# Performance work log

Hardware: AMD Instinct MI355X
Metric: run time of the kernel (lower is better)

Reference implementation:

```python
import jax, jax.numpy as jnp
import numpy as np

N_NODES = 100000
N_EDGES = 1600000
N_GRAPHS = 512
IN_CH = 128
FILT = 128
N_CONVS = 4  # 1 + n_rounds(3)


def setup_inputs() -> dict:
    key = jax.random.key(0)
    ks = jax.random.split(key, 10)
    x = jax.random.normal(ks[0], (N_NODES, IN_CH), dtype=jnp.float32)
    edge_index = jax.random.randint(ks[1], (2, N_EDGES), 0, N_NODES, dtype=jnp.int32)
    batch = jnp.sort(jax.random.randint(ks[2], (N_NODES,), 0, N_GRAPHS, dtype=jnp.int32))
    # GCNConv weights (in_channels == filter_size so all convs stack uniformly)
    s = 1.0 / np.sqrt(FILT)
    conv_w = jax.random.uniform(ks[3], (N_CONVS, IN_CH, FILT), jnp.float32, -s, s)
    conv_b = jnp.zeros((N_CONVS, FILT), jnp.float32)
    fc1_w = jax.random.uniform(ks[4], (FILT, FILT), jnp.float32, -s, s)
    fc1_b = jax.random.uniform(ks[5], (FILT,), jnp.float32, -s, s)
    fc2_w = jax.random.uniform(ks[6], (FILT, 1), jnp.float32, -s, s)
    fc2_b = jax.random.uniform(ks[7], (1,), jnp.float32, -s, s)
    return {"x": x, "edge_index": edge_index, "batch": batch, "batch_size": N_GRAPHS,
            "conv_w": conv_w, "conv_b": conv_b,
            "fc1_w": fc1_w, "fc1_b": fc1_b, "fc2_w": fc2_w, "fc2_b": fc2_b}


def _gcn_layer(x, W, b, src, dst, dinv):
    # GCNConv with improved=True: A_hat = A + 2I, sym-normalized by D_hat^{-1/2}
    h = x @ W                                   # [N, F]
    enorm = dinv[src] * dinv[dst]               # [E]
    agg = jax.ops.segment_sum(h[src] * enorm[:, None], dst, num_segments=N_NODES)
    self_loop = (2.0 * dinv * dinv)[:, None] * h
    return agg + self_loop + b


def reference(x, edge_index, batch, batch_size, conv_w, conv_b, fc1_w, fc1_b, fc2_w, fc2_b):
    src, dst = edge_index[0], edge_index[1]
    # degree including improved self-loop weight 2
    deg = jax.ops.segment_sum(jnp.ones((N_EDGES,), x.dtype), dst, num_segments=N_NODES) + 2.0
    dinv = jax.lax.rsqrt(deg)
    for i in range(N_CONVS):
        x = _gcn_layer(x, conv_w[i], conv_b[i], src, dst, dinv)
        x = jax.nn.relu(x)
        # dropout is identity in eval mode
    # global mean pool over graphs
    sums = jax.ops.segment_sum(x, batch, num_segments=batch_size)
    cnt = jax.ops.segment_sum(jnp.ones((N_NODES,), x.dtype), batch, num_segments=batch_size)
    pooled = sums / jnp.maximum(cnt, 1.0)[:, None]   # [G, F]
    h = jax.nn.relu(pooled @ fc1_w + fc1_b)
    out = h @ fc2_w + fc2_b                          # [G, 1]
    return out[:, 0]
```

## Files before the change

kernel.cpp:

```cpp
#include <hip/hip_runtime.h>
#include <hip/hip_fp16.h>

#define N_NODES 100000
#define N_EDGES 1600000
#define N_GRAPHS 512
#define F 128
#define N_CONVS 4
#define SCAN_NBLK ((N_NODES + 1023) / 1024)

#define SUBW 256
#define SUBW_NODES 391
#define SCAP 7040
#define ACHUNK 4096
#define BINA_BLOCKS ((N_EDGES + ACHUNK - 1) / ACHUNK)
#define EBUF 8192

#define W2_STRIDE 132
#define W2_LAYER (128 * W2_STRIDE)

typedef __attribute__((ext_vector_type(8))) short short8;
typedef __attribute__((ext_vector_type(4))) float f32x4;

union FragU { uint4 u; short8 v; };
union HU4 { uint4 u; __half2 h[4]; };

__device__ __forceinline__ unsigned int pack_hilo(float f) {
    unsigned int u = __float_as_uint(f);
    unsigned int hb = u & 0xFFFF0000u;
    float d = f - __uint_as_float(hb);
    unsigned int lb = __float_as_uint(d) >> 16;
    return (u >> 16) | (lb << 16);
}


__global__ void dinv_kernel(const int* __restrict__ cnt, float* __restrict__ dinv) {
    int n = blockIdx.x * blockDim.x + threadIdx.x;
    if (n < N_NODES) dinv[n] = rsqrtf((float)cnt[n] + 2.0f);
}

__global__ void scan1_kernel(const int* __restrict__ cnt, int* __restrict__ excl,
                             int* __restrict__ blksum) {
    __shared__ int sums[256];
    int t = threadIdx.x;
    int base = blockIdx.x * 1024 + t * 4;
    int v0 = 0, v1 = 0, v2 = 0, v3 = 0;
    if (base + 0 < N_NODES) v0 = cnt[base + 0];
    if (base + 1 < N_NODES) v1 = cnt[base + 1];
    if (base + 2 < N_NODES) v2 = cnt[base + 2];
    if (base + 3 < N_NODES) v3 = cnt[base + 3];
    int s = v0 + v1 + v2 + v3;
    sums[t] = s;
    __syncthreads();
    for (int off = 1; off < 256; off <<= 1) {
        int y = (t >= off) ? sums[t - off] : 0;
        __syncthreads();
        sums[t] += y;
        __syncthreads();
    }
    int pre = sums[t] - s;
    if (base + 0 < N_NODES) excl[base + 0] = pre;
    if (base + 1 < N_NODES) excl[base + 1] = pre + v0;
    if (base + 2 < N_NODES) excl[base + 2] = pre + v0 + v1;
    if (base + 3 < N_NODES) excl[base + 3] = pre + v0 + v1 + v2;
    if (t == 255) blksum[blockIdx.x] = sums[255];
}

__global__ void scan2_kernel(int* __restrict__ blksum, int nblk) {
    __shared__ int sh[128];
    int t = threadIdx.x;
    int v = (t < nblk) ? blksum[t] : 0;
    sh[t] = v;
    __syncthreads();
    for (int off = 1; off < 128; off <<= 1) {
        int y = (t >= off) ? sh[t - off] : 0;
        __syncthreads();
        sh[t] += y;
        __syncthreads();
    }
    if (t < nblk) blksum[t] = sh[t] - v;
}

__global__ void scan3_kernel(int* __restrict__ rowptr, const int* __restrict__ blksum) {
    int t = threadIdx.x;
    int base = blockIdx.x * 1024 + t * 4;
    int off = blksum[blockIdx.x];
#pragma unroll
    for (int i = 0; i < 4; i++) {
        int idx = base + i;
        if (idx < N_NODES) rowptr[idx] += off;
    }
    if (blockIdx.x == 0 && t == 0) rowptr[N_NODES] = N_EDGES;
}


__global__ __launch_bounds__(256) void binA_kernel(
        const int* __restrict__ src, const int* __restrict__ dst,
        int* __restrict__ cursor, int2* __restrict__ staging) {
    __shared__ int2 buf[ACHUNK];
    __shared__ int cnt_s[SUBW], off_s[SUBW], cur_s[SUBW], gb_s[SUBW], sh[SUBW];
    int t = threadIdx.x;
    cnt_s[t] = 0;
    __syncthreads();

    int base = blockIdx.x * ACHUNK;
    int n = N_EDGES - base;
    if (n > ACHUNK) n = ACHUNK;

    for (int li = t; li < n; li += 256)
        atomicAdd(&cnt_s[dst[base + li] / SUBW_NODES], 1);
    __syncthreads();

    int v = cnt_s[t];
    sh[t] = v;
    __syncthreads();
    for (int off = 1; off < SUBW; off <<= 1) {
        int y = (t >= off) ? sh[t - off] : 0;
        __syncthreads();
        sh[t] += y;
        __syncthreads();
    }
    int excl = sh[t] - v;
    off_s[t] = excl;
    cur_s[t] = excl;
    gb_s[t] = atomicAdd(&cursor[t], v);
    __syncthreads();

    for (int li = t; li < n; li += 256) {
        int e = base + li;
        int d = dst[e], s = src[e];
        int p = atomicAdd(&cur_s[d / SUBW_NODES], 1);
        buf[p] = make_int2(s, d);
    }
    __syncthreads();

    for (int i = t; i < n; i += 256) {
        int2 e = buf[i];
        int w = e.y / SUBW_NODES;
        int idx = gb_s[w] + (i - off_s[w]);
        if (idx < SCAP) staging[(size_t)w * SCAP + idx] = e;
    }
}

__global__ __launch_bounds__(256) void subcount_kernel(
        const int2* __restrict__ staging, const int* __restrict__ cursor,
        int* __restrict__ cnt) {
    __shared__ int hist[SUBW_NODES];
    int b = blockIdx.x, t = threadIdx.x;
    int n0 = b * SUBW_NODES;
    int n1 = n0 + SUBW_NODES;
    if (n1 > N_NODES) n1 = N_NODES;
    int nn = n1 - n0;
    for (int i = t; i < nn; i += 256) hist[i] = 0;
    __syncthreads();
    int m = cursor[b];
    if (m > SCAP) m = SCAP;
    for (int i = t; i < m; i += 256) {
        int d = staging[(size_t)b * SCAP + i].y;
        atomicAdd(&hist[d - n0], 1);
    }
    __syncthreads();
    for (int i = t; i < nn; i += 256) cnt[n0 + i] = hist[i];
}

__global__ __launch_bounds__(512) void binB_kernel(
        const int2* __restrict__ staging, const int* __restrict__ cursor,
        const int* __restrict__ rowptr, const float* __restrict__ dinv,
        int2* __restrict__ edges) {
    __shared__ int rowl[SUBW_NODES + 1];
    __shared__ int lcur[SUBW_NODES];
    __shared__ int2 ebuf[EBUF];
    int b = blockIdx.x, t = threadIdx.x;
    int n0 = b * SUBW_NODES;
    int n1 = n0 + SUBW_NODES;
    if (n1 > N_NODES) n1 = N_NODES;
    int nn = n1 - n0;

    for (int i = t; i <= nn; i += 512) rowl[i] = rowptr[n0 + i];
    for (int i = t; i < nn; i += 512) lcur[i] = 0;
    __syncthreads();

    int gb = rowl[0];
    int total = rowl[nn] - gb;
    int m = cursor[b];
    if (m > SCAP) m = SCAP;

    for (int i = t; i < m; i += 512) {
        int2 e = staging[(size_t)b * SCAP + i];
        int s = e.x, d = e.y;
        float wt = dinv[s] * dinv[d];
        int dl = d - n0;
        int lpos = (rowl[dl] - gb) + atomicAdd(&lcur[dl], 1);
        if (lpos < EBUF) ebuf[lpos] = make_int2(s, __float_as_int(wt));
    }
    __syncthreads();

    for (int i = t; i < total; i += 512)
        if (i < EBUF) edges[gb + i] = ebuf[i];
}


__global__ void wpack_kernel(const float* __restrict__ conv_w, unsigned int* __restrict__ W2g) {
    int idx = blockIdx.x * 256 + threadIdx.x;
    if (idx < N_CONVS * 16384) {
        int L = idx >> 14;
        int e = idx & 16383;
        int k = e >> 7;
        int n = e & 127;
        float f = conv_w[(size_t)L * 16384 + k * 128 + n];
        W2g[(size_t)L * W2_LAYER + n * W2_STRIDE + k] = pack_hilo(f);
    }
}


template<bool F16IN>
__global__ __launch_bounds__(256, 2) void gemm_mfma_t(const void* __restrict__ Xv,
                                                      const unsigned int* __restrict__ W2g,
                                                      __half* __restrict__ Hh) {
    __shared__ unsigned int wlds[128 * W2_STRIDE];
    int t = threadIdx.x;

    {
        const uint4* s4 = (const uint4*)W2g;
        uint4* d4 = (uint4*)wlds;
#pragma unroll
        for (int i = 0; i < 17; i++) {
            int idx = i * 256 + t;
            if (idx < (128 * W2_STRIDE) / 4) d4[idx] = s4[idx];
        }
    }
    __syncthreads();

    int w = t >> 6;
    int l = t & 63;
    int m = l & 15;
    int q = l >> 4;
    int r0 = blockIdx.x * 128 + w * 32 + m;
    int r1 = r0 + 16;
    int r0c = (r0 > N_NODES - 1) ? (N_NODES - 1) : r0;
    int r1c = (r1 > N_NODES - 1) ? (N_NODES - 1) : r1;

    uint4 a0[8], a1[8];
#pragma unroll
    for (int i = 0; i < 8; i++) {
        if constexpr (F16IN) {
            const uint2* X2 = (const uint2*)Xv;
            uint2 hv = X2[(size_t)r0c * 32 + i * 4 + q];
            float2 f0 = __half22float2(*(const __half2*)&hv.x);
            float2 f1 = __half22float2(*(const __half2*)&hv.y);
            a0[i].x = pack_hilo(f0.x); a0[i].y = pack_hilo(f0.y);
            a0[i].z = pack_hilo(f1.x); a0[i].w = pack_hilo(f1.y);
            uint2 gv = X2[(size_t)r1c * 32 + i * 4 + q];
            float2 g0 = __half22float2(*(const __half2*)&gv.x);
            float2 g1 = __half22float2(*(const __half2*)&gv.y);
            a1[i].x = pack_hilo(g0.x); a1[i].y = pack_hilo(g0.y);
            a1[i].z = pack_hilo(g1.x); a1[i].w = pack_hilo(g1.y);
        } else {
            const float4* X4 = (const float4*)Xv;
            float4 xv = X4[(size_t)r0c * 32 + i * 4 + q];
            a0[i].x = pack_hilo(xv.x); a0[i].y = pack_hilo(xv.y);
            a0[i].z = pack_hilo(xv.z); a0[i].w = pack_hilo(xv.w);
            float4 yv = X4[(size_t)r1c * 32 + i * 4 + q];
            a1[i].x = pack_hilo(yv.x); a1[i].y = pack_hilo(yv.y);
            a1[i].z = pack_hilo(yv.z); a1[i].w = pack_hilo(yv.w);
        }
    }

    f32x4 acc0[8], acc1[8];
#pragma unroll
    for (int nb = 0; nb < 8; nb++) {
        acc0[nb] = (f32x4){0.f, 0.f, 0.f, 0.f};
        acc1[nb] = (f32x4){0.f, 0.f, 0.f, 0.f};
    }

#pragma unroll
    for (int nb = 0; nb < 8; nb++) {
        const unsigned int* wb = &wlds[(nb * 16 + m) * W2_STRIDE];
#pragma unroll
        for (int i = 0; i < 8; i++) {
            uint4 b = *(const uint4*)(wb + i * 16 + q * 4);
            FragU fa0, fa1, fb, fr;
            fa0.u = a0[i]; fa1.u = a1[i]; fb.u = b;
            acc0[nb] = __builtin_amdgcn_mfma_f32_16x16x32_bf16(fa0.v, fb.v, acc0[nb], 0, 0, 0);
            acc1[nb] = __builtin_amdgcn_mfma_f32_16x16x32_bf16(fa1.v, fb.v, acc1[nb], 0, 0, 0);
            fr.u.x = (b.x >> 16) | (b.x << 16);
            fr.u.y = (b.y >> 16) | (b.y << 16);
            fr.u.z = (b.z >> 16) | (b.z << 16);
            fr.u.w = (b.w >> 16) | (b.w << 16);
            acc0[nb] = __builtin_amdgcn_mfma_f32_16x16x32_bf16(fa0.v, fr.v, acc0[nb], 0, 0, 0);
            acc1[nb] = __builtin_amdgcn_mfma_f32_16x16x32_bf16(fa1.v, fr.v, acc1[nb], 0, 0, 0);
        }
    }

    int rbase = blockIdx.x * 128 + w * 32 + q * 4;
#pragma unroll
    for (int nb = 0; nb < 8; nb++) {
#pragma unroll
        for (int r = 0; r < 4; r++) {
            int row = rbase + r;
            if (row < N_NODES) Hh[(size_t)row * F + nb * 16 + m] = __float2half(acc0[nb][r]);
            int row1 = row + 16;
            if (row1 < N_NODES) Hh[(size_t)row1 * F + nb * 16 + m] = __float2half(acc1[nb][r]);
        }
    }
}


__global__ __launch_bounds__(256) void agg_kernel(const uint4* __restrict__ H16,
                                                  const int* __restrict__ rowptr,
                                                  const int2* __restrict__ edges,
                                                  const float* __restrict__ dinv,
                                                  const float4* __restrict__ bias4,
                                                  uint4* __restrict__ Xo) {
    int node = blockIdx.x * 4 + (threadIdx.x >> 6);
    if (node >= N_NODES) return;
    int lane = threadIdx.x & 63;
    int c16 = lane & 15;
    int slot = lane >> 4;

    int lo = rowptr[node];
    int hi = rowptr[node + 1];
    int him1 = hi - 1;

    float4 aL = make_float4(0.f, 0.f, 0.f, 0.f);
    float4 aH = make_float4(0.f, 0.f, 0.f, 0.f);

    for (int i = lo + slot; i < hi; i += 16) {
        int s[4]; float w[4]; uint4 v[4];
#pragma unroll
        for (int j = 0; j < 4; j++) {
            int ij = i + 4 * j;
            int cj = (ij < him1) ? ij : him1;
            int2 e = edges[cj];
            s[j] = e.x;
            w[j] = (ij < hi) ? __int_as_float(e.y) : 0.f;
        }
#pragma unroll
        for (int j = 0; j < 4; j++) v[j] = H16[(size_t)s[j] * 16 + c16];
#pragma unroll
        for (int j = 0; j < 4; j++) {
            HU4 x; x.u = v[j];
            float2 p0 = __half22float2(x.h[0]);
            float2 p1 = __half22float2(x.h[1]);
            float2 p2 = __half22float2(x.h[2]);
            float2 p3 = __half22float2(x.h[3]);
            aL.x = fmaf(w[j], p0.x, aL.x); aL.y = fmaf(w[j], p0.y, aL.y);
            aL.z = fmaf(w[j], p1.x, aL.z); aL.w = fmaf(w[j], p1.y, aL.w);
            aH.x = fmaf(w[j], p2.x, aH.x); aH.y = fmaf(w[j], p2.y, aH.y);
            aH.z = fmaf(w[j], p3.x, aH.z); aH.w = fmaf(w[j], p3.y, aH.w);
        }
    }

    aL.x += __shfl_down(aL.x, 32, 64); aL.y += __shfl_down(aL.y, 32, 64);
    aL.z += __shfl_down(aL.z, 32, 64); aL.w += __shfl_down(aL.w, 32, 64);
    aH.x += __shfl_down(aH.x, 32, 64); aH.y += __shfl_down(aH.y, 32, 64);
    aH.z += __shfl_down(aH.z, 32, 64); aH.w += __shfl_down(aH.w, 32, 64);
    aL.x += __shfl_down(aL.x, 16, 64); aL.y += __shfl_down(aL.y, 16, 64);
    aL.z += __shfl_down(aL.z, 16, 64); aL.w += __shfl_down(aL.w, 16, 64);
    aH.x += __shfl_down(aH.x, 16, 64); aH.y += __shfl_down(aH.y, 16, 64);
    aH.z += __shfl_down(aH.z, 16, 64); aH.w += __shfl_down(aH.w, 16, 64);

    if (slot == 0) {
        float dn = dinv[node];
        float sw = 2.0f * dn * dn;
        HU4 x; x.u = H16[(size_t)node * 16 + c16];
        float2 p0 = __half22float2(x.h[0]);
        float2 p1 = __half22float2(x.h[1]);
        float2 p2 = __half22float2(x.h[2]);
        float2 p3 = __half22float2(x.h[3]);
        float4 bL = bias4[c16 * 2];
        float4 bH = bias4[c16 * 2 + 1];
        float4 rL, rH;
        rL.x = fmaxf(fmaf(sw, p0.x, aL.x) + bL.x, 0.f);
        rL.y = fmaxf(fmaf(sw, p0.y, aL.y) + bL.y, 0.f);
        rL.z = fmaxf(fmaf(sw, p1.x, aL.z) + bL.z, 0.f);
        rL.w = fmaxf(fmaf(sw, p1.y, aL.w) + bL.w, 0.f);
        rH.x = fmaxf(fmaf(sw, p2.x, aH.x) + bH.x, 0.f);
        rH.y = fmaxf(fmaf(sw, p2.y, aH.y) + bH.y, 0.f);
        rH.z = fmaxf(fmaf(sw, p3.x, aH.z) + bH.z, 0.f);
        rH.w = fmaxf(fmaf(sw, p3.y, aH.w) + bH.w, 0.f);
        HU4 o;
        o.h[0] = __floats2half2_rn(rL.x, rL.y);
        o.h[1] = __floats2half2_rn(rL.z, rL.w);
        o.h[2] = __floats2half2_rn(rH.x, rH.y);
        o.h[3] = __floats2half2_rn(rH.z, rH.w);
        Xo[(size_t)node * 16 + c16] = o.u;
    }
}


__global__ __launch_bounds__(256) void pool_fc_kernel(const __half* __restrict__ x,
                                                      const int* __restrict__ batch,
                                                      const float* __restrict__ fc1w,
                                                      const float* __restrict__ fc1b,
                                                      const float* __restrict__ fc2w,
                                                      const float* __restrict__ fc2b,
                                                      float* __restrict__ out) {
    __shared__ float part[2][F];
    __shared__ float pooled[F];
    __shared__ int bnd[2];
    __shared__ float red[2];
    int g = blockIdx.x, t = threadIdx.x;
    int c = t & 127, hlf = t >> 7;

    if (t < 2) {
        int target = g + t;
        int lo = 0, hi = N_NODES;
        while (lo < hi) {
            int m = (lo + hi) >> 1;
            if (batch[m] < target) lo = m + 1;
            else hi = m;
        }
        bnd[t] = lo;
    }
    __syncthreads();
    int lo = bnd[0], hi = bnd[1];

    float s = 0.f;
    int n = lo + hlf;
    for (; n + 6 < hi; n += 8) {
        float v0 = __half2float(x[(size_t)n * F + c]);
        float v1 = __half2float(x[(size_t)(n + 2) * F + c]);
        float v2 = __half2float(x[(size_t)(n + 4) * F + c]);
        float v3 = __half2float(x[(size_t)(n + 6) * F + c]);
        s += (v0 + v1) + (v2 + v3);
    }
    for (; n < hi; n += 2) s += __half2float(x[(size_t)n * F + c]);
    part[hlf][c] = s;
    __syncthreads();

    if (t < F) {
        float cntf = fmaxf((float)(hi - lo), 1.0f);
        pooled[c] = (part[0][c] + part[1][c]) / cntf;
    }
    __syncthreads();

    if (t < F) {
        float acc = fc1b[t];
#pragma unroll 4
        for (int k = 0; k < F; k++) acc = fmaf(pooled[k], fc1w[k * F + t], acc);
        acc = fmaxf(acc, 0.f);

        float p = acc * fc2w[t];
#pragma unroll
        for (int o = 32; o > 0; o >>= 1) p += __shfl_down(p, o, 64);
        if ((t & 63) == 0) red[t >> 6] = p;
    }
    __syncthreads();
    if (t == 0) out[g] = red[0] + red[1] + fc2b[0];
}


extern "C" void kernel_launch(void* const* d_in, const int* in_sizes, int n_in,
                              void* d_out, int out_size, void* d_ws, size_t ws_size,
                              hipStream_t stream) {
    const float* x_in   = (const float*)d_in[0];
    const int*   eidx   = (const int*)d_in[1];
    const int*   batch  = (const int*)d_in[2];
    const float* conv_w = (const float*)d_in[4];
    const float* conv_b = (const float*)d_in[5];
    const float* fc1w   = (const float*)d_in[6];
    const float* fc1b   = (const float*)d_in[7];
    const float* fc2w   = (const float*)d_in[8];
    const float* fc2b   = (const float*)d_in[9];
    float* out = (float*)d_out;

    const int* src = eidx;
    const int* dst = eidx + N_EDGES;

    char* ws = (char*)d_ws;
    size_t off = 0;
    auto alloc = [&](size_t bytes) -> char* {
        char* p = ws + off;
        off += (bytes + 255) & ~(size_t)255;
        return p;
    };
    __half* bufA  = (__half*)alloc((size_t)N_NODES * F * 2);
    __half* bufH  = (__half*)alloc((size_t)N_NODES * F * 2);
    float*  dinv  = (float*)alloc((size_t)N_NODES * 4);
    int*    cnt   = (int*)alloc((size_t)N_NODES * 4);
    int*    rowp  = (int*)alloc((size_t)(N_NODES + 1) * 4);
    int2*   edges = (int2*)alloc((size_t)N_EDGES * 8);
    unsigned int* W2g = (unsigned int*)alloc((size_t)N_CONVS * W2_LAYER * 4);
    int*    blks  = (int*)alloc(128 * 4);
    int*    cursor = (int*)alloc(SUBW * 4);
    int2*   staging = (int2*)alloc((size_t)SUBW * SCAP * 8);
    (void)ws_size; (void)in_sizes; (void)n_in; (void)out_size;

    hipMemsetAsync(cursor, 0, SUBW * 4, stream);
    binA_kernel<<<BINA_BLOCKS, 256, 0, stream>>>(src, dst, cursor, staging);
    subcount_kernel<<<SUBW, 256, 0, stream>>>(staging, cursor, cnt);

    dinv_kernel<<<(N_NODES + 255) / 256, 256, 0, stream>>>(cnt, dinv);
    scan1_kernel<<<SCAN_NBLK, 256, 0, stream>>>(cnt, rowp, blks);
    scan2_kernel<<<1, 128, 0, stream>>>(blks, SCAN_NBLK);
    scan3_kernel<<<SCAN_NBLK, 256, 0, stream>>>(rowp, blks);
    wpack_kernel<<<(N_CONVS * 16384 + 255) / 256, 256, 0, stream>>>(conv_w, W2g);

    binB_kernel<<<SUBW, 512, 0, stream>>>(staging, cursor, rowp, dinv, edges);

    for (int L = 0; L < N_CONVS; L++) {
        if (L == 0)
            gemm_mfma_t<false><<<(N_NODES + 127) / 128, 256, 0, stream>>>(
                (const void*)x_in, W2g, bufH);
        else
            gemm_mfma_t<true><<<(N_NODES + 127) / 128, 256, 0, stream>>>(
                (const void*)bufA, W2g + (size_t)L * W2_LAYER, bufH);
        agg_kernel<<<(N_NODES + 3) / 4, 256, 0, stream>>>(
            (const uint4*)bufH, rowp, edges, dinv,
            (const float4*)(conv_b + (size_t)L * F), (uint4*)bufA);
    }

    pool_fc_kernel<<<N_GRAPHS, 256, 0, stream>>>(bufA, batch, fc1w, fc1b, fc2w, fc2b, out);
}
```

Before: 518.5 us.

## Store node features in column-blocked layout and split aggregation by channel block

Hidden features now live in eight column blocks of 16 channels, each laid out node-major, instead of row-major over all 128 channels. GEMM reads and writes, the pool kernel, and a new aggregation kernel are all updated to that layout. Each aggregation block handles one 16-channel slice for 8 nodes, with 32 lanes per node and 2 lanes per edge. The intent is to make each slice's gather working set (100k nodes × 32 B) small enough to stay in cache across neighbor reads. The cost is that edge lists and rowptr are read eight times, and each gather is only 16 B per lane, down from unrolled groups of 4 loads.

```diff
diff --git a/kernel.cpp b/kernel.cpp
--- a/kernel.cpp
+++ b/kernel.cpp
@@ -14,6 +14,9 @@
 #define ACHUNK 4096
 #define BINA_BLOCKS ((N_EDGES + ACHUNK - 1) / ACHUNK)
 #define EBUF 8192
+
+#define AGG_NODES_PER_BLK 8
+#define AGG_CHUNKS ((N_NODES + AGG_NODES_PER_BLK - 1) / AGG_NODES_PER_BLK)
 
 #define W2_STRIDE 132
 #define W2_LAYER (128 * W2_STRIDE)
@@ -244,12 +247,12 @@
     for (int i = 0; i < 8; i++) {
         if constexpr (F16IN) {
             const uint2* X2 = (const uint2*)Xv;
-            uint2 hv = X2[(size_t)r0c * 32 + i * 4 + q];
+            uint2 hv = X2[((size_t)i * N_NODES + r0c) * 4 + q];
             float2 f0 = __half22float2(*(const __half2*)&hv.x);
             float2 f1 = __half22float2(*(const __half2*)&hv.y);
             a0[i].x = pack_hilo(f0.x); a0[i].y = pack_hilo(f0.y);
             a0[i].z = pack_hilo(f1.x); a0[i].w = pack_hilo(f1.y);
-            uint2 gv = X2[(size_t)r1c * 32 + i * 4 + q];
+            uint2 gv = X2[((size_t)i * N_NODES + r1c) * 4 + q];
             float2 g0 = __half22float2(*(const __half2*)&gv.x);
             float2 g1 = __half22float2(*(const __half2*)&gv.y);
             a1[i].x = pack_hilo(g0.x); a1[i].y = pack_hilo(g0.y);
@@ -297,93 +300,86 @@
 #pragma unroll
         for (int r = 0; r < 4; r++) {
             int row = rbase + r;
-            if (row < N_NODES) Hh[(size_t)row * F + nb * 16 + m] = __float2half(acc0[nb][r]);
+            if (row < N_NODES)
+                Hh[((size_t)nb * N_NODES + row) * 16 + m] = __float2half(acc0[nb][r]);
             int row1 = row + 16;
-            if (row1 < N_NODES) Hh[(size_t)row1 * F + nb * 16 + m] = __float2half(acc1[nb][r]);
+            if (row1 < N_NODES)
+                Hh[((size_t)nb * N_NODES + row1) * 16 + m] = __float2half(acc1[nb][r]);
         }
     }
 }
 
 
-__global__ __launch_bounds__(256) void agg_kernel(const uint4* __restrict__ H16,
-                                                  const int* __restrict__ rowptr,
-                                                  const int2* __restrict__ edges,
-                                                  const float* __restrict__ dinv,
-                                                  const float4* __restrict__ bias4,
-                                                  uint4* __restrict__ Xo) {
-    int node = blockIdx.x * 4 + (threadIdx.x >> 6);
+__global__ __launch_bounds__(256) void aggb_kernel(const uint4* __restrict__ Hq,
+                                                   const int* __restrict__ rowptr,
+                                                   const int2* __restrict__ edges,
+                                                   const float* __restrict__ dinv,
+                                                   const float4* __restrict__ bias4,
+                                                   uint4* __restrict__ Xo) {
+    int cb = blockIdx.x & 7;
+    int chunk = blockIdx.x >> 3;
+    int lane = threadIdx.x & 63;
+    int wv = threadIdx.x >> 6;
+    int node = chunk * AGG_NODES_PER_BLK + wv * 2 + (lane >> 5);
     if (node >= N_NODES) return;
-    int lane = threadIdx.x & 63;
-    int c16 = lane & 15;
-    int slot = lane >> 4;
+    int l5 = lane & 31;
+    int slot = l5 >> 1;
+    int half = lane & 1;
+    size_t cbase = (size_t)cb * N_NODES;
 
     int lo = rowptr[node];
     int hi = rowptr[node + 1];
-    int him1 = hi - 1;
-
-    float4 aL = make_float4(0.f, 0.f, 0.f, 0.f);
-    float4 aH = make_float4(0.f, 0.f, 0.f, 0.f);
+
+    float4 a0 = make_float4(0.f, 0.f, 0.f, 0.f);
+    float4 a1 = make_float4(0.f, 0.f, 0.f, 0.f);
 
     for (int i = lo + slot; i < hi; i += 16) {
-        int s[4]; float w[4]; uint4 v[4];
-#pragma unroll
-        for (int j = 0; j < 4; j++) {
-            int ij = i + 4 * j;
-            int cj = (ij < him1) ? ij : him1;
-            int2 e = edges[cj];
-            s[j] = e.x;
-            w[j] = (ij < hi) ? __int_as_float(e.y) : 0.f;
-        }
-#pragma unroll
-        for (int j = 0; j < 4; j++) v[j] = H16[(size_t)s[j] * 16 + c16];
-#pragma unroll
-        for (int j = 0; j < 4; j++) {
-            HU4 x; x.u = v[j];
-            float2 p0 = __half22float2(x.h[0]);
-            float2 p1 = __half22float2(x.h[1]);
-            float2 p2 = __half22float2(x.h[2]);
-            float2 p3 = __half22float2(x.h[3]);
-            aL.x = fmaf(w[j], p0.x, aL.x); aL.y = fmaf(w[j], p0.y, aL.y);
-            aL.z = fmaf(w[j], p1.x, aL.z); aL.w = fmaf(w[j], p1.y, aL.w);
-            aH.x = fmaf(w[j], p2.x, aH.x); aH.y = fmaf(w[j], p2.y, aH.y);
-            aH.z = fmaf(w[j], p3.x, aH.z); aH.w = fmaf(w[j], p3.y, aH.w);
-        }
-    }
-
-    aL.x += __shfl_down(aL.x, 32, 64); aL.y += __shfl_down(aL.y, 32, 64);
-    aL.z += __shfl_down(aL.z, 32, 64); aL.w += __shfl_down(aL.w, 32, 64);
-    aH.x += __shfl_down(aH.x, 32, 64); aH.y += __shfl_down(aH.y, 32, 64);
-    aH.z += __shfl_down(aH.z, 32, 64); aH.w += __shfl_down(aH.w, 32, 64);
-    aL.x += __shfl_down(aL.x, 16, 64); aL.y += __shfl_down(aL.y, 16, 64);
-    aL.z += __shfl_down(aL.z, 16, 64); aL.w += __shfl_down(aL.w, 16, 64);
-    aH.x += __shfl_down(aH.x, 16, 64); aH.y += __shfl_down(aH.y, 16, 64);
-    aH.z += __shfl_down(aH.z, 16, 64); aH.w += __shfl_down(aH.w, 16, 64);
-
-    if (slot == 0) {
-        float dn = dinv[node];
-        float sw = 2.0f * dn * dn;
-        HU4 x; x.u = H16[(size_t)node * 16 + c16];
+        int2 e = edges[i];
+        float w = __int_as_float(e.y);
+        HU4 x; x.u = Hq[(cbase + e.x) * 2 + half];
         float2 p0 = __half22float2(x.h[0]);
         float2 p1 = __half22float2(x.h[1]);
         float2 p2 = __half22float2(x.h[2]);
         float2 p3 = __half22float2(x.h[3]);
-        float4 bL = bias4[c16 * 2];
-        float4 bH = bias4[c16 * 2 + 1];
+        a0.x = fmaf(w, p0.x, a0.x); a0.y = fmaf(w, p0.y, a0.y);
+        a0.z = fmaf(w, p1.x, a0.z); a0.w = fmaf(w, p1.y, a0.w);
+        a1.x = fmaf(w, p2.x, a1.x); a1.y = fmaf(w, p2.y, a1.y);
+        a1.z = fmaf(w, p3.x, a1.z); a1.w = fmaf(w, p3.y, a1.w);
+    }
+
+#pragma unroll
+    for (int d = 16; d >= 2; d >>= 1) {
+        a0.x += __shfl_down(a0.x, d, 64); a0.y += __shfl_down(a0.y, d, 64);
+        a0.z += __shfl_down(a0.z, d, 64); a0.w += __shfl_down(a0.w, d, 64);
+        a1.x += __shfl_down(a1.x, d, 64); a1.y += __shfl_down(a1.y, d, 64);
+        a1.z += __shfl_down(a1.z, d, 64); a1.w += __shfl_down(a1.w, d, 64);
+    }
+
+    if (slot == 0) {
+        float dn = dinv[node];
+        float sw = 2.0f * dn * dn;
+        HU4 x; x.u = Hq[(cbase + node) * 2 + half];
+        float2 p0 = __half22float2(x.h[0]);
+        float2 p1 = __half22float2(x.h[1]);
+        float2 p2 = __half22float2(x.h[2]);
+        float2 p3 = __half22float2(x.h[3]);
+        float4 bL = bias4[cb * 4 + half * 2];
+        float4 bH = bias4[cb * 4 + half * 2 + 1];
         float4 rL, rH;
-        rL.x = fmaxf(fmaf(sw, p0.x, aL.x) + bL.x, 0.f);
-        rL.y = fmaxf(fmaf(sw, p0.y, aL.y) + bL.y, 0.f);
-        rL.z = fmaxf(fmaf(sw, p1.x, aL.z) + bL.z, 0.f);
-        rL.w = fmaxf(fmaf(sw, p1.y, aL.w) + bL.w, 0.f);
-        rH.x = fmaxf(fmaf(sw, p2.x, aH.x) + bH.x, 0.f);
-        rH.y = fmaxf(fmaf(sw, p2.y, aH.y) + bH.y, 0.f);
-        rH.z = fmaxf(fmaf(sw, p3.x, aH.z) + bH.z, 0.f);
-        rH.w = fmaxf(fmaf(sw, p3.y, aH.w) + bH.w, 0.f);
+        rL.x = fmaxf(fmaf(sw, p0.x, a0.x) + bL.x, 0.f);
+        rL.y = fmaxf(fmaf(sw, p0.y, a0.y) + bL.y, 0.f);
+        rL.z = fmaxf(fmaf(sw, p1.x, a0.z) + bL.z, 0.f);
+        rL.w = fmaxf(fmaf(sw, p1.y, a0.w) + bL.w, 0.f);
+        rH.x = fmaxf(fmaf(sw, p2.x, a1.x) + bH.x, 0.f);
+        rH.y = fmaxf(fmaf(sw, p2.y, a1.y) + bH.y, 0.f);
+        rH.z = fmaxf(fmaf(sw, p3.x, a1.z) + bH.z, 0.f);
+        rH.w = fmaxf(fmaf(sw, p3.y, a1.w) + bH.w, 0.f);
         HU4 o;
         o.h[0] = __floats2half2_rn(rL.x, rL.y);
         o.h[1] = __floats2half2_rn(rL.z, rL.w);
         o.h[2] = __floats2half2_rn(rH.x, rH.y);
         o.h[3] = __floats2half2_rn(rH.z, rH.w);
-        Xo[(size_t)node * 16 + c16] = o.u;
+        Xo[(cbase + node) * 2 + half] = o.u;
     }
 }
 
@@ -415,16 +411,18 @@
     __syncthreads();
     int lo = bnd[0], hi = bnd[1];
 
+    size_t cboff = ((size_t)(c >> 4) * N_NODES) * 16 + (c & 15);
+
     float s = 0.f;
     int n = lo + hlf;
     for (; n + 6 < hi; n += 8) {
-        float v0 = __half2float(x[(size_t)n * F + c]);
-        float v1 = __half2float(x[(size_t)(n + 2) * F + c]);
-        float v2 = __half2float(x[(size_t)(n + 4) * F + c]);
-        float v3 = __half2float(x[(size_t)(n + 6) * F + c]);
+        float v0 = __half2float(x[cboff + (size_t)n * 16]);
+        float v1 = __half2float(x[cboff + (size_t)(n + 2) * 16]);
+        float v2 = __half2float(x[cboff + (size_t)(n + 4) * 16]);
+        float v3 = __half2float(x[cboff + (size_t)(n + 6) * 16]);
         s += (v0 + v1) + (v2 + v3);
     }
-    for (; n < hi; n += 2) s += __half2float(x[(size_t)n * F + c]);
+    for (; n < hi; n += 2) s += __half2float(x[cboff + (size_t)n * 16]);
     part[hlf][c] = s;
     __syncthreads();
 
@@ -505,7 +503,7 @@
         else
             gemm_mfma_t<true><<<(N_NODES + 127) / 128, 256, 0, stream>>>(
                 (const void*)bufA, W2g + (size_t)L * W2_LAYER, bufH);
-        agg_kernel<<<(N_NODES + 3) / 4, 256, 0, stream>>>(
+        aggb_kernel<<<AGG_CHUNKS * 8, 256, 0, stream>>>(
             (const uint4*)bufH, rowp, edges, dinv,
             (const float4*)(conv_b + (size_t)L * F), (uint4*)bufA);
     }
```

New measurement: 848.4 us. 63.6% more time.

## Split feature matrix into two 64-channel planes for cache-friendlier aggregation

Applied to the files above, without the earlier changes.

Stores the fp16 hidden features as two column-halves, each a contiguous [N,64] plane, and changes the GEMM, aggregation and pooling kernels to match. The aggregation kernel now processes one channel half per block, with two nodes per wavefront and four edge slots each, so each gather touches a 128-byte row segment. Consecutive blocks work on the two halves of the same nodes. The intent is a smaller gather working set per pass for better L2 reuse, at the cost of reading edge lists twice and launching twice as many blocks.

```diff
diff --git a/kernel.cpp b/kernel.cpp
--- a/kernel.cpp
+++ b/kernel.cpp
@@ -14,6 +14,8 @@
 #define ACHUNK 4096
 #define BINA_BLOCKS ((N_EDGES + ACHUNK - 1) / ACHUNK)
 #define EBUF 8192
+
+#define AGG64_BLOCKS ((N_NODES / 8) * 2)
 
 #define W2_STRIDE 132
 #define W2_LAYER (128 * W2_STRIDE)
@@ -244,12 +246,12 @@
     for (int i = 0; i < 8; i++) {
         if constexpr (F16IN) {
             const uint2* X2 = (const uint2*)Xv;
-            uint2 hv = X2[(size_t)r0c * 32 + i * 4 + q];
+            uint2 hv = X2[((size_t)(i >> 2) * N_NODES + r0c) * 16 + (i & 3) * 4 + q];
             float2 f0 = __half22float2(*(const __half2*)&hv.x);
             float2 f1 = __half22float2(*(const __half2*)&hv.y);
             a0[i].x = pack_hilo(f0.x); a0[i].y = pack_hilo(f0.y);
             a0[i].z = pack_hilo(f1.x); a0[i].w = pack_hilo(f1.y);
-            uint2 gv = X2[(size_t)r1c * 32 + i * 4 + q];
+            uint2 gv = X2[((size_t)(i >> 2) * N_NODES + r1c) * 16 + (i & 3) * 4 + q];
             float2 g0 = __half22float2(*(const __half2*)&gv.x);
             float2 g1 = __half22float2(*(const __half2*)&gv.y);
             a1[i].x = pack_hilo(g0.x); a1[i].y = pack_hilo(g0.y);
@@ -297,25 +299,33 @@
 #pragma unroll
         for (int r = 0; r < 4; r++) {
             int row = rbase + r;
-            if (row < N_NODES) Hh[(size_t)row * F + nb * 16 + m] = __float2half(acc0[nb][r]);
+            if (row < N_NODES)
+                Hh[((size_t)(nb >> 2) * N_NODES + row) * 64 + (nb & 3) * 16 + m]
+                    = __float2half(acc0[nb][r]);
             int row1 = row + 16;
-            if (row1 < N_NODES) Hh[(size_t)row1 * F + nb * 16 + m] = __float2half(acc1[nb][r]);
-        }
-    }
-}
-
-
-__global__ __launch_bounds__(256) void agg_kernel(const uint4* __restrict__ H16,
-                                                  const int* __restrict__ rowptr,
-                                                  const int2* __restrict__ edges,
-                                                  const float* __restrict__ dinv,
-                                                  const float4* __restrict__ bias4,
-                                                  uint4* __restrict__ Xo) {
-    int node = blockIdx.x * 4 + (threadIdx.x >> 6);
-    if (node >= N_NODES) return;
+            if (row1 < N_NODES)
+                Hh[((size_t)(nb >> 2) * N_NODES + row1) * 64 + (nb & 3) * 16 + m]
+                    = __float2half(acc1[nb][r]);
+        }
+    }
+}
+
+
+__global__ __launch_bounds__(256) void agg64_kernel(const uint4* __restrict__ Hq,
+                                                    const int* __restrict__ rowptr,
+                                                    const int2* __restrict__ edges,
+                                                    const float* __restrict__ dinv,
+                                                    const float4* __restrict__ bias4,
+                                                    uint4* __restrict__ Xo) {
+    int cb = blockIdx.x & 1;
+    int grp = blockIdx.x >> 1;
     int lane = threadIdx.x & 63;
-    int c16 = lane & 15;
-    int slot = lane >> 4;
+    int wv = threadIdx.x >> 6;
+    int nsub = lane >> 5;
+    int slot = (lane >> 3) & 3;
+    int c8 = lane & 7;
+    int node = grp * 8 + wv * 2 + nsub;
+    size_t cbase = (size_t)cb * N_NODES;
 
     int lo = rowptr[node];
     int hi = rowptr[node + 1];
@@ -335,7 +345,7 @@
             w[j] = (ij < hi) ? __int_as_float(e.y) : 0.f;
         }
 #pragma unroll
-        for (int j = 0; j < 4; j++) v[j] = H16[(size_t)s[j] * 16 + c16];
+        for (int j = 0; j < 4; j++) v[j] = Hq[(cbase + s[j]) * 8 + c8];
 #pragma unroll
         for (int j = 0; j < 4; j++) {
             HU4 x; x.u = v[j];
@@ -350,25 +360,25 @@
         }
     }
 
-    aL.x += __shfl_down(aL.x, 32, 64); aL.y += __shfl_down(aL.y, 32, 64);
-    aL.z += __shfl_down(aL.z, 32, 64); aL.w += __shfl_down(aL.w, 32, 64);
-    aH.x += __shfl_down(aH.x, 32, 64); aH.y += __shfl_down(aH.y, 32, 64);
-    aH.z += __shfl_down(aH.z, 32, 64); aH.w += __shfl_down(aH.w, 32, 64);
     aL.x += __shfl_down(aL.x, 16, 64); aL.y += __shfl_down(aL.y, 16, 64);
     aL.z += __shfl_down(aL.z, 16, 64); aL.w += __shfl_down(aL.w, 16, 64);
     aH.x += __shfl_down(aH.x, 16, 64); aH.y += __shfl_down(aH.y, 16, 64);
     aH.z += __shfl_down(aH.z, 16, 64); aH.w += __shfl_down(aH.w, 16, 64);
+    aL.x += __shfl_down(aL.x, 8, 64); aL.y += __shfl_down(aL.y, 8, 64);
+    aL.z += __shfl_down(aL.z, 8, 64); aL.w += __shfl_down(aL.w, 8, 64);
+    aH.x += __shfl_down(aH.x, 8, 64); aH.y += __shfl_down(aH.y, 8, 64);
+    aH.z += __shfl_down(aH.z, 8, 64); aH.w += __shfl_down(aH.w, 8, 64);
 
     if (slot == 0) {
         float dn = dinv[node];
         float sw = 2.0f * dn * dn;
-        HU4 x; x.u = H16[(size_t)node * 16 + c16];
+        HU4 x; x.u = Hq[(cbase + node) * 8 + c8];
         float2 p0 = __half22float2(x.h[0]);
         float2 p1 = __half22float2(x.h[1]);
         float2 p2 = __half22float2(x.h[2]);
         float2 p3 = __half22float2(x.h[3]);
-        float4 bL = bias4[c16 * 2];
-        float4 bH = bias4[c16 * 2 + 1];
+        float4 bL = bias4[cb * 16 + c8 * 2];
+        float4 bH = bias4[cb * 16 + c8 * 2 + 1];
         float4 rL, rH;
         rL.x = fmaxf(fmaf(sw, p0.x, aL.x) + bL.x, 0.f);
         rL.y = fmaxf(fmaf(sw, p0.y, aL.y) + bL.y, 0.f);
@@ -383,7 +393,7 @@
         o.h[1] = __floats2half2_rn(rL.z, rL.w);
         o.h[2] = __floats2half2_rn(rH.x, rH.y);
         o.h[3] = __floats2half2_rn(rH.z, rH.w);
-        Xo[(size_t)node * 16 + c16] = o.u;
+        Xo[(cbase + node) * 8 + c8] = o.u;
     }
 }
 
@@ -415,16 +425,18 @@
     __syncthreads();
     int lo = bnd[0], hi = bnd[1];
 
+    size_t cboff = ((size_t)(c >> 6) * N_NODES) * 64 + (c & 63);
+
     float s = 0.f;
     int n = lo + hlf;
     for (; n + 6 < hi; n += 8) {
-        float v0 = __half2float(x[(size_t)n * F + c]);
-        float v1 = __half2float(x[(size_t)(n + 2) * F + c]);
-        float v2 = __half2float(x[(size_t)(n + 4) * F + c]);
-        float v3 = __half2float(x[(size_t)(n + 6) * F + c]);
+        float v0 = __half2float(x[cboff + (size_t)n * 64]);
+        float v1 = __half2float(x[cboff + (size_t)(n + 2) * 64]);
+        float v2 = __half2float(x[cboff + (size_t)(n + 4) * 64]);
+        float v3 = __half2float(x[cboff + (size_t)(n + 6) * 64]);
         s += (v0 + v1) + (v2 + v3);
     }
-    for (; n < hi; n += 2) s += __half2float(x[(size_t)n * F + c]);
+    for (; n < hi; n += 2) s += __half2float(x[cboff + (size_t)n * 64]);
     part[hlf][c] = s;
     __syncthreads();
 
@@ -505,7 +517,7 @@
         else
             gemm_mfma_t<true><<<(N_NODES + 127) / 128, 256, 0, stream>>>(
                 (const void*)bufA, W2g + (size_t)L * W2_LAYER, bufH);
-        agg_kernel<<<(N_NODES + 3) / 4, 256, 0, stream>>>(
+        agg64_kernel<<<AGG64_BLOCKS, 256, 0, stream>>>(
             (const uint4*)bufH, rowp, edges, dinv,
             (const float4*)(conv_b + (size_t)L * F), (uint4*)bufA);
     }
```

Result: no change. 510.3 us (-1.6%).
